# Kernel tuning notes

Hardware: AMD Instinct MI355X
Metric: run time of the kernel (lower is better)

## Reference

```python
import jax, jax.numpy as jnp
import numpy as np

B, T, N, F = 16, 12, 1024, 8
H = 64        # hidden_size
K = 2         # diffusion order (DCRNN k == DiffConv gnn_kernel)
HORIZON = 12
E = 32 * N    # number of edges


def setup_inputs() -> dict:
    key = jax.random.key(0)
    ks = jax.random.split(key, 16)
    s = 0.05
    inp = {}
    inp['x'] = jax.random.normal(ks[0], (B, T, N, F), jnp.float32)
    inp['edge_index'] = jax.random.randint(ks[1], (2, E), 0, N)
    inp['edge_weight'] = jax.random.uniform(ks[2], (E,), jnp.float32)
    inp['adj'] = jax.random.uniform(ks[3], (N, N), jnp.float32)
    # encoder Linear(F -> H)
    inp['W_enc'] = jax.random.normal(ks[4], (F, H), jnp.float32) * s
    inp['b_enc'] = jnp.zeros((H,), jnp.float32)
    # NodeEmbedding(n_nodes, H)
    inp['node_emb'] = jax.random.normal(ks[5], (N, H), jnp.float32) * s
    # DCRNN gates: DenseGraphConvOrderK(2H -> H), 2 supports x K hops (include_self=False)
    gin = 2 * H * 2 * K
    inp['W_r'] = jax.random.normal(ks[6], (gin, H), jnp.float32) * s
    inp['b_r'] = jnp.zeros((H,), jnp.float32)
    inp['W_u'] = jax.random.normal(ks[7], (gin, H), jnp.float32) * s
    inp['b_u'] = jnp.zeros((H,), jnp.float32)
    inp['W_c'] = jax.random.normal(ks[8], (gin, H), jnp.float32) * s
    inp['b_c'] = jnp.zeros((H,), jnp.float32)
    # DiffConv filters: Linear(H*(2K+1) -> H), root_weight=True, add_backward=True
    din = H * (2 * K + 1)
    inp['W_diff'] = jax.random.normal(ks[9], (din, H), jnp.float32) * s
    inp['b_diff'] = jnp.zeros((H,), jnp.float32)
    # decoder Linear(H -> F*HORIZON)
    inp['W_dec'] = jax.random.normal(ks[10], (H, F * HORIZON), jnp.float32) * s
    inp['b_dec'] = jnp.zeros((F * HORIZON,), jnp.float32)
    return inp


def _dgconv(x, supports, W, b):
    # DenseGraphConvOrderK, include_self=False: for each support, K hop powers, concat on channels.
    feats = []
    for a in supports:  # a: [n, n], row-normalized transition matrix
        x1 = x
        for _ in range(K):
            x1 = jnp.einsum('bvc,wv->bwc', x1, a)
            feats.append(x1)
    return jnp.concatenate(feats, axis=-1) @ W + b


def _forward(x, edge_index, edge_weight, adj, W_enc, b_enc, node_emb,
             W_r, b_r, W_u, b_u, W_c, b_c, W_diff, b_diff, W_dec, b_dec):
    # --- DenseGraphConvOrderK.compute_support: fwd/bwd row-normalized transitions ---
    adj_fwd = adj / adj.sum(1, keepdims=True)
    adjT = adj.T
    adj_bwd = adjT / adjT.sum(1, keepdims=True)
    supports = (adj_fwd, adj_bwd)

    # encoder + node embeddings (broadcast over batch & time)
    x_enc = x @ W_enc + b_enc + node_emb  # [B, T, N, H]

    # --- DenseDCRNN: GRU with diffusion-conv gates, scan over time ---
    def step(h, xt):
        xh = jnp.concatenate([xt, h], axis=-1)                 # [B, N, 2H]
        r = jax.nn.sigmoid(_dgconv(xh, supports, W_r, b_r))    # forget/reset gate
        u = jax.nn.sigmoid(_dgconv(xh, supports, W_u, b_u))    # update gate
        xc = jnp.concatenate([xt, r * h], axis=-1)
        c = jnp.tanh(_dgconv(xc, supports, W_c, b_c))          # candidate
        h_new = u * h + (1.0 - u) * c
        return h_new, None

    h0 = jnp.zeros((B, N, H), x_enc.dtype)
    h, _ = jax.lax.scan(step, h0, jnp.swapaxes(x_enc, 0, 1))   # last state, [B, N, H]

    # --- DiffConv readout on sparse edge list (root + K fwd hops + K bwd hops) ---
    src, dst = edge_index[0], edge_index[1]

    def norm_w(group_idx):
        deg = jax.ops.segment_sum(edge_weight, group_idx, num_segments=N)
        inv = jnp.where(deg > 0, 1.0 / deg, 0.0)
        return edge_weight * inv[group_idx]

    w_fwd = norm_w(dst)  # normalize over target (dim=1)
    w_bwd = norm_w(src)  # flipped edges, normalized over their targets (= src)

    feats = [h]
    for s_, d_, w_ in ((src, dst, w_fwd), (dst, src, w_bwd)):
        xs = h
        for _ in range(K):
            msg = xs[:, s_, :] * w_[None, :, None]             # [B, E, H]
            xs = jnp.zeros_like(h).at[:, d_, :].add(msg)
            feats.append(xs)
    z = jnp.concatenate(feats, axis=-1) @ W_diff + b_diff      # [B, N, H]

    # decoder + rearrange 'b n (t f) -> b t n f'
    out = z @ W_dec + b_dec                                    # [B, N, HORIZON*F]
    return out.reshape(B, N, HORIZON, F).transpose(0, 2, 1, 3) # [B, HORIZON, N, F]


def reference(x, edge_index, edge_weight, adj, W_enc, b_enc, node_emb,
              W_r, b_r, W_u, b_u, W_c, b_c, W_diff, b_diff, W_dec, b_dec):
    return _forward(x, edge_index, edge_weight, adj, W_enc, b_enc, node_emb,
                    W_r, b_r, W_u, b_u, W_c, b_c, W_diff, b_diff, W_dec, b_dec)
```

## Files before the change

kernel.cpp:

```cpp
#include <hip/hip_runtime.h>
#include <math.h>

#define BB 16
#define TT 12
#define NN 1024
#define FF 8
#define HH 64
#define EE 32768
#define DIN 320
#define ODIM 96
#define APAD 40

typedef _Float16 v8h __attribute__((ext_vector_type(8)));
typedef float v4f __attribute__((ext_vector_type(4)));

__device__ __forceinline__ unsigned short f2h(float v) {
    _Float16 h = (_Float16)v;
    unsigned short u;
    __builtin_memcpy(&u, &h, 2);
    return u;
}
__device__ __forceinline__ float h2f(unsigned short u) {
    _Float16 h;
    __builtin_memcpy(&h, &u, 2);
    return (float)h;
}
__device__ __forceinline__ void gl_lds16(const void* g, void* l) {
    __builtin_amdgcn_global_load_lds(
        (const __attribute__((address_space(1))) unsigned int*)g,
        (__attribute__((address_space(3))) unsigned int*)l, 16, 0, 0);
}

__global__ void k_ei_detect(const int* __restrict__ ei_raw, int* __restrict__ flag) {
    __shared__ int s[256];
    s[threadIdx.x] = ei_raw[2 * threadIdx.x + 1];
    __syncthreads();
    for (int st = 128; st > 0; st >>= 1) {
        if (threadIdx.x < st) s[threadIdx.x] |= s[threadIdx.x + st];
        __syncthreads();
    }
    if (threadIdx.x == 0) flag[0] = (s[0] == 0) ? 1 : 0;
}
__global__ void k_ei_norm(const int* __restrict__ ei_raw, const int* __restrict__ flag,
                          int* __restrict__ ei32) {
    int j = blockIdx.x * 256 + threadIdx.x;
    ei32[j] = flag[0] ? ei_raw[2 * j] : ei_raw[j];
}

__global__ void k_rowsum(const float* __restrict__ adj, float* __restrict__ rinv) {
    __shared__ float s[256];
    int i = blockIdx.x;
    float acc = 0.f;
    for (int j = threadIdx.x; j < NN; j += 256) acc += adj[i * NN + j];
    s[threadIdx.x] = acc;
    __syncthreads();
    for (int st = 128; st > 0; st >>= 1) {
        if (threadIdx.x < st) s[threadIdx.x] += s[threadIdx.x + st];
        __syncthreads();
    }
    if (threadIdx.x == 0) rinv[i] = (s[0] != 0.f) ? 1.f / s[0] : 0.f;
}
__global__ void k_colsumP(const float* __restrict__ adj, float* __restrict__ csum) {
    int bi = blockIdx.x;
    int j4 = threadIdx.x * 4;
    float4 acc = {0.f, 0.f, 0.f, 0.f};
    const float* base = adj + (size_t)bi * 16 * NN + j4;
    #pragma unroll
    for (int r = 0; r < 16; r++) {
        float4 v = *(const float4*)(base + (size_t)r * NN);
        acc.x += v.x; acc.y += v.y; acc.z += v.z; acc.w += v.w;
    }
    atomicAdd(&csum[j4 + 0], acc.x);
    atomicAdd(&csum[j4 + 1], acc.y);
    atomicAdd(&csum[j4 + 2], acc.z);
    atomicAdd(&csum[j4 + 3], acc.w);
}
__global__ void k_cinv(const float* __restrict__ csum, float* __restrict__ cinv) {
    int j = blockIdx.x * 256 + threadIdx.x;
    float s = csum[j];
    cinv[j] = (s != 0.f) ? 1.f / s : 0.f;
}

__global__ __launch_bounds__(256) void k_prepA(
        const float* __restrict__ adj, const float* __restrict__ rinv,
        const float* __restrict__ cinv, unsigned short* __restrict__ Mp) {
    int w0 = blockIdx.x * 64, v0 = blockIdx.y * 64;
    __shared__ float T[64][68];
    int row = threadIdx.x >> 2, cs = (threadIdx.x & 3) * 16;
    #pragma unroll
    for (int j = 0; j < 4; j++)
        *(float4*)&T[row][cs + j * 4] = *(const float4*)(adj + (size_t)(w0 + row) * NN + v0 + cs + j * 4);
    __syncthreads();
    {
        float sc = rinv[w0 + row];
        unsigned short h8[16];
        #pragma unroll
        for (int j = 0; j < 16; j++) h8[j] = f2h(T[row][cs + j] * sc);
        size_t ofs = (size_t)(w0 + row) * NN + v0 + cs;
        ((uint4*)(Mp + ofs))[0] = *(uint4*)&h8[0];
        ((uint4*)(Mp + ofs))[1] = *(uint4*)&h8[8];
    }
    {
        float sc = cinv[v0 + row];
        unsigned short h8[16];
        #pragma unroll
        for (int j = 0; j < 16; j++) h8[j] = f2h(T[cs + j][row] * sc);
        size_t ofs = (size_t)2048 * NN + (size_t)(v0 + row) * NN + w0 + cs;
        ((uint4*)(Mp + ofs))[0] = *(uint4*)&h8[0];
        ((uint4*)(Mp + ofs))[1] = *(uint4*)&h8[8];
    }
}

__global__ __launch_bounds__(256) void k_msq(unsigned short* __restrict__ M) {
    int zz = blockIdx.z;
    size_t srcb = (size_t)zz * 2048 * NN;
    size_t dstb = srcb + (size_t)1024 * NN;
    int w0 = blockIdx.x * 64, n0 = blockIdx.y * 64;

    __shared__ unsigned short sA[64 * APAD];
    __shared__ unsigned short sB[64 * APAD];

    int tid = threadIdx.x;
    int lane = tid & 63, wave = tid >> 6;
    int wr = (wave >> 1) * 32, wc = (wave & 1) * 32;
    int l15 = lane & 15, quad = lane >> 4;
    int arow = tid >> 2, akk = (tid & 3) * 8;
    int bkr = tid & 31, bc8 = (tid >> 5) * 8;

    v4f acc[2][2];
    #pragma unroll
    for (int i = 0; i < 2; i++)
        #pragma unroll
        for (int j = 0; j < 2; j++) { acc[i][j][0]=0.f; acc[i][j][1]=0.f; acc[i][j][2]=0.f; acc[i][j][3]=0.f; }

    for (int k0 = 0; k0 < NN; k0 += 32) {
        *(uint4*)&sA[arow * APAD + akk] = *(const uint4*)(M + srcb + (size_t)(w0 + arow) * NN + k0 + akk);
        uint4 bh = *(const uint4*)(M + srcb + (size_t)(k0 + bkr) * NN + n0 + bc8);
        const unsigned short* ph = (const unsigned short*)&bh;
        #pragma unroll
        for (int j = 0; j < 8; j++) sB[(bc8 + j) * APAD + bkr] = ph[j];
        __syncthreads();

        v8h a0 = *(const v8h*)&sA[(wr + l15) * APAD + quad * 8];
        v8h a1 = *(const v8h*)&sA[(wr + 16 + l15) * APAD + quad * 8];
        #pragma unroll
        for (int j = 0; j < 2; j++) {
            v8h bb = *(const v8h*)&sB[(wc + j * 16 + l15) * APAD + quad * 8];
            acc[0][j] = __builtin_amdgcn_mfma_f32_16x16x32_f16(a0, bb, acc[0][j], 0, 0, 0);
            acc[1][j] = __builtin_amdgcn_mfma_f32_16x16x32_f16(a1, bb, acc[1][j], 0, 0, 0);
        }
        __syncthreads();
    }

    #pragma unroll
    for (int i = 0; i < 2; i++)
        #pragma unroll
        for (int j = 0; j < 2; j++) {
            int rb = w0 + wr + i * 16 + quad * 4;
            int cc = n0 + wc + j * 16 + l15;
            #pragma unroll
            for (int rr = 0; rr < 4; rr++)
                M[dstb + (size_t)(rb + rr) * NN + cc] = f2h(acc[i][j][rr]);
        }
}

__global__ void k_m2frag(const unsigned short* __restrict__ P, unsigned short* __restrict__ F) {
    size_t t = (size_t)blockIdx.x * 256 + threadIdx.x;
    int rowloc = (int)(t & 63);
    int kc = (int)((t >> 6) & 127);
    int T = (int)(t >> 13);
    size_t src = ((size_t)(T * 64 + rowloc) * NN) + kc * 8;
    *(uint4*)(F + t * 8) = *(const uint4*)(P + src);
}

__global__ void k_xT(const float* __restrict__ x, unsigned short* __restrict__ XallT) {
    int bx = blockIdx.x;
    int t = bx >> 4, b = bx & 15;
    int tid = threadIdx.x;
    int f = tid & 7, half = tid >> 3;
    const float* xs = x + ((size_t)b * TT + t) * NN * FF + f;
    int n0 = half * 32;
    unsigned short v[32];
    #pragma unroll
    for (int i = 0; i < 32; i++) v[i] = f2h(xs[(size_t)(n0 + i) * FF]);
    unsigned short* dst = XallT + ((size_t)bx * 8 + f) * NN + n0;
    #pragma unroll
    for (int i = 0; i < 4; i++) *(uint4*)(dst + i * 8) = *(uint4*)&v[i * 8];
}
__global__ void k_embT(const float* __restrict__ emb, unsigned short* __restrict__ XallT) {
    int c = blockIdx.x;
    int n0 = threadIdx.x * 4;
    unsigned short v[4];
    #pragma unroll
    for (int j = 0; j < 4; j++) v[j] = f2h(emb[(size_t)(n0 + j) * HH + c]);
    *(uint2*)(XallT + (size_t)(1536 + c) * NN + n0) = *(uint2*)v;
}

__global__ __launch_bounds__(512) void k_hopX(
        const unsigned short* __restrict__ Mf,
        const unsigned short* __restrict__ XallT,
        unsigned short* __restrict__ AX, unsigned short* __restrict__ Eg) {
    int bid = blockIdx.x;
    int rt = bid & 31;
    int y  = bid >> 5;
    int g = rt >> 3;
    int n0 = (rt & 7) * 128;
    int c0 = y * 128;

    __shared__ unsigned short sA[2][16 * 512];
    __shared__ unsigned short sX[2][16 * 512];

    int tid = threadIdx.x;
    int lane = tid & 63, wave = tid >> 6;
    int rh = wave >> 2, cq = wave & 3;
    int l15 = lane & 15, quad = lane >> 4;

    v4f acc[4][2];
    #pragma unroll
    for (int i = 0; i < 4; i++)
        #pragma unroll
        for (int j = 0; j < 2; j++) { acc[i][j][0]=0.f; acc[i][j][1]=0.f; acc[i][j][2]=0.f; acc[i][j][3]=0.f; }

    auto STAGE = [&](int buf, int k0) {
        #pragma unroll
        for (int s = 0; s < 4; s++) {
            int id = wave + s * 8;
            if (id < 16) {
                int ah = id >> 3, kh = (id >> 2) & 1, rf = id & 3;
                const unsigned short* src = Mf +
                    ((size_t)(rt * 2 + ah) * 8192 +
                     (size_t)((k0 >> 3) + kh * 4 + quad) * 64 + rf * 16 + l15) * 8;
                gl_lds16(src, &sA[buf][id * 512]);
            } else {
                int xi = id - 16, cj = xi >> 1, kh = xi & 1;
                const unsigned short* src = XallT +
                    (size_t)(c0 + cj * 16 + l15) * NN + k0 + kh * 32 + quad * 8;
                gl_lds16(src, &sX[buf][xi * 512]);
            }
        }
    };

    STAGE(0, 0);
    STAGE(1, 64);

    int lu = lane * 8;
// ... 41 lines not shown
                }
            }
        }
}

__global__ void k_veg(const float* __restrict__ W_enc,
                      const float* __restrict__ W_r, const float* __restrict__ W_u,
                      const float* __restrict__ W_c, float* __restrict__ Veg) {
    int idx = blockIdx.x * 256 + threadIdx.x;
    int c = idx & 63;
    int gf = (idx >> 6) & 31;
    int G = idx >> 11;
    int g = gf >> 3, f = gf & 7;
    const float* W = (G == 0) ? W_r : ((G == 1) ? W_u : W_c);
    float acc = 0.f;
    for (int c2 = 0; c2 < 64; c2++)
        acc += W_enc[f * HH + c2] * W[(size_t)(g * 128 + c2) * HH + c];
    Veg[idx] = acc;
}

__global__ void k_constE(const unsigned short* __restrict__ Eg, const float* __restrict__ b_enc,
                         const float* __restrict__ W_r, const float* __restrict__ W_u,
                         const float* __restrict__ W_c, float* __restrict__ constE) {
    int G = blockIdx.y;
    int n = blockIdx.x * 4 + (threadIdx.x >> 6);
    int c = threadIdx.x & 63;
    const float* W = (G == 0) ? W_r : ((G == 1) ? W_u : W_c);
    float acc = 0.f;
    for (int g = 0; g < 4; g++)
        for (int c2 = 0; c2 < 64; c2++)
            acc += (h2f(Eg[((size_t)(g << 10) + n) * 64 + c2]) + b_enc[c2]) *
                   W[(size_t)(g * 128 + c2) * HH + c];
    constE[((size_t)G << 16) + (size_t)n * 64 + c] = acc;
}

__global__ void k_wfragH(const float* __restrict__ W_r, const float* __restrict__ W_u,
                         const float* __restrict__ W_c,
                         unsigned short* __restrict__ Fr, unsigned short* __restrict__ Fu,
                         unsigned short* __restrict__ Fc) {
    int idx = blockIdx.x * 256 + threadIdx.x;
    int G = idx >> 14;
    int r = idx & 16383;
    int e = r & 7, l = (r >> 3) & 63;
    int rest = r >> 9;
    int ks = rest & 7, cj = rest >> 3;
    int c = cj * 16 + (l & 15);
    int k = ks * 32 + (l >> 4) * 8 + e;
    int g = k >> 6, c2 = k & 63;
    const float* W = (G == 0) ? W_r : ((G == 1) ? W_u : W_c);
    unsigned short* F = (G == 0) ? Fr : ((G == 1) ? Fu : Fc);
    F[r] = f2h(W[(size_t)(g * 128 + 64 + c2) * HH + c]);
}
__global__ void k_wfragX(const float* __restrict__ Veg, unsigned short* __restrict__ Wx) {
    int idx = blockIdx.x * 256 + threadIdx.x;
    int G = idx >> 11;
    int r = idx & 2047;
    int e = r & 7, l = (r >> 3) & 63;
    int cj = r >> 9;
    int c = cj * 16 + (l & 15);
    int k = (l >> 4) * 8 + e;
    Wx[idx] = f2h(Veg[(size_t)G * 2048 + (size_t)k * 64 + c]);
}

__global__ void k_wfragO(const float* __restrict__ W_diff, const float* __restrict__ W_dec,
                         unsigned short* __restrict__ Wf) {
    int idx = blockIdx.x * 256 + threadIdx.x;
    int e = idx & 7, l = (idx >> 3) & 63;
    int rest = idx >> 9;
    int ks = rest % 10, cj = rest / 10;
    int o = cj * 16 + (l & 15);
    int k = ks * 32 + (l >> 4) * 8 + e;
    float acc = 0.f;
    for (int c = 0; c < 64; c++) acc += W_diff[(size_t)k * HH + c] * W_dec[(size_t)c * ODIM + o];
    Wf[idx] = f2h(acc);
}
__global__ void k_bzd(const float* __restrict__ b_diff, const float* __restrict__ W_dec,
                      const float* __restrict__ b_dec, float* __restrict__ bzd) {
    int o = threadIdx.x;
    float acc = b_dec[o];
    for (int c = 0; c < 64; c++) acc += b_diff[c] * W_dec[(size_t)c * ODIM + o];
    bzd[o] = acc;
}

__global__ __launch_bounds__(512) void k_hopRU(
        const unsigned short* __restrict__ Mf,
        const unsigned short* __restrict__ XhH,
        const unsigned short* __restrict__ AXt,
        const unsigned short* __restrict__ WfrH, const unsigned short* __restrict__ WfuH,
        const unsigned short* __restrict__ Wxr, const unsigned short* __restrict__ Wxu,
        const float* __restrict__ b_r, const float* __restrict__ b_u,
        const float* __restrict__ constE,
        const float* __restrict__ h,
        unsigned short* __restrict__ XhR, float* __restrict__ ubuf) {
    int bid = blockIdx.x;
    int b = bid >> 5, nth = bid & 31;
    int nt = nth >> 1, hb = nth & 1;
    int n0 = nth * 32;

    __shared__ unsigned short S[2][24 * 512];

    int tid = threadIdx.x;
    int lane = tid & 63, wave = tid >> 6;
    int l15 = lane & 15, quad = lane >> 4;
    int g = wave >> 1, rh = wave & 1;

    const unsigned short* Xbase = XhH + (size_t)b * 64 * NN;

    v4f acc[4];
    #pragma unroll
    for (int j = 0; j < 4; j++) { acc[j][0]=0.f; acc[j][1]=0.f; acc[j][2]=0.f; acc[j][3]=0.f; }

    auto STAGE = [&](int buf, int k0) {
        #pragma unroll
        for (int s = 0; s < 3; s++) {
            int id = wave + s * 8;
            if (id < 16) {
                int gg = id >> 2, kh = (id >> 1) & 1, rfi = id & 1;
                int rf = hb * 2 + rfi;
                const unsigned short* src = Mf +
                    ((size_t)(gg * 16 + nt) * 8192 +
                     (size_t)((k0 >> 3) + kh * 4 + quad) * 64 + rf * 16 + l15) * 8;
                gl_lds16(src, &S[buf][id * 512]);
            } else {
                int xi = id - 16, cj = xi >> 1, kh = xi & 1;
                const unsigned short* src = Xbase +
                    (size_t)(cj * 16 + l15) * NN + k0 + kh * 32 + quad * 8;
                gl_lds16(src, &S[buf][id * 512]);
            }
        }
    };

    STAGE(0, 0);
    STAGE(1, 64);

    int lu = lane * 8;
    for (int kt = 0; kt < 16; kt++) {
        int cur = kt & 1;
        if (kt < 15) asm volatile("s_waitcnt vmcnt(3)" ::: "memory");
        else         asm volatile("s_waitcnt vmcnt(0)" ::: "memory");
        __builtin_amdgcn_s_barrier();
        asm volatile("" ::: "memory");
        #pragma unroll
        for (int kh = 0; kh < 2; kh++) {
            v8h a = *(const v8h*)&S[cur][(g * 4 + kh * 2 + rh) * 512 + lu];
            #pragma unroll
            for (int cj = 0; cj < 4; cj++) {
                v8h bx = *(const v8h*)&S[cur][(16 + cj * 2 + kh) * 512 + lu];
                acc[cj] = __builtin_amdgcn_mfma_f32_16x16x32_f16(a, bx, acc[cj], 0, 0, 0);
            }
        }
        asm volatile("" ::: "memory");
        __builtin_amdgcn_s_barrier();
        asm volatile("" ::: "memory");
        if (kt < 14) STAGE(cur, (kt + 2) * 64);
    }

    unsigned short* Yt = &S[0][0];
    #pragma unroll
    for (int cj = 0; cj < 4; cj++) {
        int col = g * 64 + cj * 16 + l15;
        #pragma unroll
        for (int rr = 0; rr < 4; rr++) {
            int row = rh * 16 + quad * 4 + rr;
            Yt[row * 264 + col] = f2h(acc[cj][rr]);
        }
    }
    __syncthreads();

    int gate = wave >> 2, rw = (wave >> 1) & 1, ch = wave & 1;
    const unsigned short* WH = gate ? WfuH : WfrH;
    const unsigned short* WX = gate ? Wxu : Wxr;
    const float* bias = gate ? b_u : b_r;
    const float* cE = constE + ((size_t)gate << 16);

    v4f acc2[2];
    #pragma unroll
    for (int j = 0; j < 2; j++) { acc2[j][0]=0.f; acc2[j][1]=0.f; acc2[j][2]=0.f; acc2[j][3]=0.f; }

    {
        v8h ax = *(const v8h*)(AXt + ((size_t)(b << 10) + n0 + rw * 16 + l15) * 32 + quad * 8);
        #pragma unroll
        for (int j = 0; j < 2; j++) {
            v8h bf = *(const v8h*)(WX + (size_t)(ch * 2 + j) * 512 + lu);
            acc2[j] = __builtin_amdgcn_mfma_f32_16x16x32_f16(ax, bf, acc2[j], 0, 0, 0);
        }
    }
    #pragma unroll
    for (int ks = 0; ks < 8; ks++) {
        v8h a = *(const v8h*)&Yt[(rw * 16 + l15) * 264 + ks * 32 + quad * 8];
        #pragma unroll
        for (int j = 0; j < 2; j++) {
            v8h bf = *(const v8h*)(WH + (size_t)((ch * 2 + j) * 8 + ks) * 512 + lu);
            acc2[j] = __builtin_amdgcn_mfma_f32_16x16x32_f16(a, bf, acc2[j], 0, 0, 0);
        }
    }

    unsigned short* sT = &S[1][0];
    if (gate == 0) {
        #pragma unroll
        for (int j = 0; j < 2; j++) {
            int c = (ch * 2 + j) * 16 + l15;
            float bb = bias[c];
            #pragma unroll
            for (int rr = 0; rr < 4; rr++) {
                int nl = rw * 16 + quad * 4 + rr;
                size_t row = (size_t)(b << 10) + n0 + nl;
                float pre = acc2[j][rr] + bb + cE[(size_t)(n0 + nl) * 64 + c];
                float r = 1.f / (1.f + expf(-pre));
                sT[c * 36 + nl] = f2h(r * h[row * 64 + c]);
            }
        }
    } else {
        #pragma unroll
        for (int j = 0; j < 2; j++) {
            int c = (ch * 2 + j) * 16 + l15;
            float bb = bias[c];
            #pragma unroll
            for (int rr = 0; rr < 4; rr++) {
                int nl = rw * 16 + quad * 4 + rr;
                size_t row = (size_t)(b << 10) + n0 + nl;
                float pre = acc2[j][rr] + bb + cE[(size_t)(n0 + nl) * 64 + c];
                ubuf[row * 64 + c] = 1.f / (1.f + expf(-pre));
            }
        }
    }
    __syncthreads();
    {
        int c = tid >> 3, n4 = (tid & 7) * 4;
        *(uint2*)(XhR + ((size_t)b * 64 + c) * NN + n0 + n4) = *(uint2*)&sT[c * 36 + n4];
    }
}

__global__ __launch_bounds__(512) void k_hopC(
        const unsigned short* __restrict__ Mf,
        const unsigned short* __restrict__ XhR,
        const unsigned short* __restrict__ AXt,
        const unsigned short* __restrict__ WfcH, const unsigned short* __restrict__ Wxc,
        const float* __restrict__ b_c,
        const float* __restrict__ constE,
        const float* __restrict__ ubuf,
        float* __restrict__ h, unsigned short* __restrict__ XhH) {
    int bid = blockIdx.x;
    int b = bid >> 5, nth = bid & 31;
    int nt = nth >> 1, hb = nth & 1;
    int n0 = nth * 32;

    __shared__ unsigned short S[2][24 * 512];

    int tid = threadIdx.x;
    int lane = tid & 63, wave = tid >> 6;
    int l15 = lane & 15, quad = lane >> 4;
    int g = wave >> 1, rh = wave & 1;

    const unsigned short* Xbase = XhR + (size_t)b * 64 * NN;

    v4f acc[4];
    #pragma unroll
    for (int j = 0; j < 4; j++) { acc[j][0]=0.f; acc[j][1]=0.f; acc[j][2]=0.f; acc[j][3]=0.f; }

    auto STAGE = [&](int buf, int k0) {
        #pragma unroll
        for (int s = 0; s < 3; s++) {
            int id = wave + s * 8;
            if (id < 16) {
                int gg = id >> 2, kh = (id >> 1) & 1, rfi = id & 1;
                int rf = hb * 2 + rfi;
                const unsigned short* src = Mf +
                    ((size_t)(gg * 16 + nt) * 8192 +
                     (size_t)((k0 >> 3) + kh * 4 + quad) * 64 + rf * 16 + l15) * 8;
                gl_lds16(src, &S[buf][id * 512]);
            } else {
                int xi = id - 16, cj = xi >> 1, kh = xi & 1;
                const unsigned short* src = Xbase +
                    (size_t)(cj * 16 + l15) * NN + k0 + kh * 32 + quad * 8;
                gl_lds16(src, &S[buf][id * 512]);
            }
        }
    };

    STAGE(0, 0);
    STAGE(1, 64);

    int lu = lane * 8;
    for (int kt = 0; kt < 16; kt++) {
        int cur = kt & 1;
        if (kt < 15) asm volatile("s_waitcnt vmcnt(3)" ::: "memory");
        else         asm volatile("s_waitcnt vmcnt(0)" ::: "memory");
        __builtin_amdgcn_s_barrier();
        asm volatile("" ::: "memory");
        #pragma unroll
        for (int kh = 0; kh < 2; kh++) {
            v8h a = *(const v8h*)&S[cur][(g * 4 + kh * 2 + rh) * 512 + lu];
            #pragma unroll
            for (int cj = 0; cj < 4; cj++) {
                v8h bx = *(const v8h*)&S[cur][(16 + cj * 2 + kh) * 512 + lu];
                acc[cj] = __builtin_amdgcn_mfma_f32_16x16x32_f16(a, bx, acc[cj], 0, 0, 0);
            }
        }
        asm volatile("" ::: "memory");
        __builtin_amdgcn_s_barrier();
        asm volatile("" ::: "memory");
        if (kt < 14) STAGE(cur, (kt + 2) * 64);
    }

    unsigned short* Yt = &S[0][0];
    #pragma unroll
    for (int cj = 0; cj < 4; cj++) {
        int col = g * 64 + cj * 16 + l15;
        #pragma unroll
        for (int rr = 0; rr < 4; rr++) {
            int row = rh * 16 + quad * 4 + rr;
            Yt[row * 264 + col] = f2h(acc[cj][rr]);
        }
    }
    __syncthreads();

    int ch = wave >> 1, rw = wave & 1;
    const float* cE = constE + ((size_t)2 << 16);

    v4f acc2;
    acc2[0]=0.f; acc2[1]=0.f; acc2[2]=0.f; acc2[3]=0.f;

    {
        v8h ax = *(const v8h*)(AXt + ((size_t)(b << 10) + n0 + rw * 16 + l15) * 32 + quad * 8);
        v8h bf = *(const v8h*)(Wxc + (size_t)ch * 512 + lu);
        acc2 = __builtin_amdgcn_mfma_f32_16x16x32_f16(ax, bf, acc2, 0, 0, 0);
    }
    #pragma unroll
    for (int ks = 0; ks < 8; ks++) {
        v8h a = *(const v8h*)&Yt[(rw * 16 + l15) * 264 + ks * 32 + quad * 8];
        v8h bf = *(const v8h*)(WfcH + (size_t)(ch * 8 + ks) * 512 + lu);
        acc2 = __builtin_amdgcn_mfma_f32_16x16x32_f16(a, bf, acc2, 0, 0, 0);
    }

    unsigned short* sT = &S[1][0];
    {
        int c = ch * 16 + l15;
        float bb = b_c[c];
        #pragma unroll
        for (int rr = 0; rr < 4; rr++) {
            int nl = rw * 16 + quad * 4 + rr;
            size_t row = (size_t)(b << 10) + n0 + nl;
            float pre = acc2[rr] + bb + cE[(size_t)(n0 + nl) * 64 + c];
            float cv = tanhf(pre);
            float u = ubuf[row * 64 + c];
            float hv = h[row * 64 + c];
            float hn = u * hv + (1.f - u) * cv;
            h[row * 64 + c] = hn;
            sT[c * 36 + nl] = f2h(hn);
        }
    }
    __syncthreads();
    {
        int c = tid >> 3, n4 = (tid & 7) * 4;
        *(uint2*)(XhH + ((size_t)b * 64 + c) * NN + n0 + n4) = *(uint2*)&sT[c * 36 + n4];
    }
}

__global__ __launch_bounds__(512) void k_hopA(
        const unsigned short* __restrict__ Mf,
        const unsigned short* __restrict__ Xb,
        unsigned short* __restrict__ Yout, int out_stride, int out_gmul, int out_off) {
    int bid = blockIdx.x;
    int rt = bid & 31;
    int bp = bid >> 5;
    int g = rt >> 3;
    int n0 = (rt & 7) * 128;

    __shared__ unsigned short sA[2][16 * 512];
    __shared__ unsigned short sX[2][16 * 512];

    int tid = threadIdx.x;
    int lane = tid & 63, wave = tid >> 6;
    int rh = wave >> 2, cq = wave & 3;
    int l15 = lane & 15, quad = lane >> 4;

    const unsigned short* Xbase = Xb + (size_t)(bp * 2) * 64 * NN;

    v4f acc[4][2];
    #pragma unroll
    for (int i = 0; i < 4; i++)
        #pragma unroll
        for (int j = 0; j < 2; j++) { acc[i][j][0]=0.f; acc[i][j][1]=0.f; acc[i][j][2]=0.f; acc[i][j][3]=0.f; }

    auto STAGE = [&](int buf, int k0) {
        #pragma unroll
        for (int s = 0; s < 4; s++) {
            int id = wave + s * 8;
            if (id < 16) {
                int ah = id >> 3, kh = (id >> 2) & 1, rf = id & 3;
                const unsigned short* src = Mf +
                    ((size_t)(rt * 2 + ah) * 8192 +
                     (size_t)((k0 >> 3) + kh * 4 + quad) * 64 + rf * 16 + l15) * 8;
                gl_lds16(src, &sA[buf][id * 512]);
            } else {
                int xi = id - 16, cj = xi >> 1, kh = xi & 1;
                const unsigned short* src = Xbase +
                    (size_t)(cj * 16 + l15) * NN + k0 + kh * 32 + quad * 8;
                gl_lds16(src, &sX[buf][xi * 512]);
            }
        }
    };

    STAGE(0, 0);
    STAGE(1, 64);

    int lu = lane * 8;
    for (int kt = 0; kt < 16; kt++) {
        int cur = kt & 1;
        if (kt < 15) asm volatile("s_waitcnt vmcnt(4)" ::: "memory");
        else         asm volatile("s_waitcnt vmcnt(0)" ::: "memory");
        __builtin_amdgcn_s_barrier();
        asm volatile("" ::: "memory");
        #pragma unroll
        for (int kh = 0; kh < 2; kh++) {
            v8h a[4], bx[2];
            #pragma unroll
            for (int rf = 0; rf < 4; rf++)
                a[rf] = *(const v8h*)&sA[cur][(rh * 8 + kh * 4 + rf) * 512 + lu];
            #pragma unroll
            for (int j = 0; j < 2; j++)
                bx[j] = *(const v8h*)&sX[cur][((cq * 2 + j) * 2 + kh) * 512 + lu];
            #pragma unroll
            for (int rf = 0; rf < 4; rf++)
                #pragma unroll
                for (int j = 0; j < 2; j++)
                    acc[rf][j] = __builtin_amdgcn_mfma_f32_16x16x32_f16(a[rf], bx[j], acc[rf][j], 0, 0, 0);
        }
        asm volatile("" ::: "memory");
        __builtin_amdgcn_s_barrier();
        asm volatile("" ::: "memory");
        if (kt < 14) STAGE(cur, (kt + 2) * 64);
    }

    #pragma unroll
    for (int rf = 0; rf < 4; rf++)
        #pragma unroll
        for (int j = 0; j < 2; j++) {
// ... 30 lines not shown
            acc[cj] = __builtin_amdgcn_mfma_f32_16x16x32_f16(a, bf, acc[cj], 0, 0, 0);
        }
    }
    #pragma unroll
    for (int cj = 0; cj < 6; cj++) {
        int o = cj * 16 + l15;
        int t = o >> 3, f = o & 7;
        float bb = bzd[o];
        #pragma unroll
        for (int rr = 0; rr < 4; rr++) {
            int row = row0 + wave * 16 + quad * 4 + rr;
            int b = row >> 10, n = row & 1023;
            out[(((size_t)b * TT + t) * NN + n) * FF + f] = acc[cj][rr] + bb;
        }
    }
}

__global__ void k_deg(const int* __restrict__ ei32, const float* __restrict__ ew,
                      float* __restrict__ degd, float* __restrict__ degs) {
    int e = blockIdx.x * 256 + threadIdx.x;
    float w = ew[e];
    atomicAdd(&degd[ei32[EE + e]], w);
    atomicAdd(&degs[ei32[e]], w);
}
__global__ void k_spadd(const int* __restrict__ ei32, const float* __restrict__ ew,
                        const float* __restrict__ degd, const float* __restrict__ degs,
                        float* __restrict__ temp) {
    int e = blockIdx.x * 256 + threadIdx.x;
    int s = ei32[e], d = ei32[EE + e];
    float w = ew[e];
    float dd = degd[d], ds = degs[s];
    float wfv = dd > 0.f ? w / dd : 0.f;
    float wbv = ds > 0.f ? w / ds : 0.f;
    atomicAdd(&temp[(size_t)d * NN + s], wfv);
    atomicAdd(&temp[(size_t)NN * NN + (size_t)s * NN + d], wbv);
}
__global__ void k_spconv(const float* __restrict__ temp, unsigned short* __restrict__ Mp) {
    size_t i0 = ((size_t)blockIdx.x * 256 + threadIdx.x) * 8;
    size_t dst = (i0 < (size_t)NN * NN) ? i0 : i0 + (size_t)NN * NN;
    unsigned short h8[8];
    #pragma unroll
    for (int j = 0; j < 8; j++) h8[j] = f2h(temp[i0 + j]);
    *(uint4*)(Mp + dst) = *(uint4*)h8;
}

__global__ void k_featd_h(const float* __restrict__ h, unsigned short* __restrict__ featd) {
    size_t idx = (size_t)blockIdx.x * 256 + threadIdx.x;
    size_t row = idx >> 6; int c = (int)(idx & 63);
    featd[row * DIN + c] = f2h(h[idx]);
}

extern "C" void kernel_launch(void* const* d_in, const int* in_sizes, int n_in,
                              void* d_out, int out_size, void* d_ws, size_t ws_size,
                              hipStream_t stream) {
    const float* x      = (const float*)d_in[0];
    const int*   eiraw  = (const int*)  d_in[1];
    const float* ew     = (const float*)d_in[2];
    const float* adj    = (const float*)d_in[3];
    const float* W_enc  = (const float*)d_in[4];
    const float* b_enc  = (const float*)d_in[5];
    const float* emb    = (const float*)d_in[6];
    const float* W_r    = (const float*)d_in[7];
    const float* b_r    = (const float*)d_in[8];
    const float* W_u    = (const float*)d_in[9];
    const float* b_u    = (const float*)d_in[10];
    const float* W_c    = (const float*)d_in[11];
    const float* b_c    = (const float*)d_in[12];
    const float* W_diff = (const float*)d_in[13];
    const float* b_diff = (const float*)d_in[14];
    const float* W_dec  = (const float*)d_in[15];
    const float* b_dec  = (const float*)d_in[16];

    unsigned short* Mf    = (unsigned short*)d_ws;
    unsigned short* XhH   = Mf + (size_t)4096 * NN;
    unsigned short* XhR   = XhH + (size_t)BB * 64 * NN;
    unsigned short* featd = XhR + (size_t)BB * 64 * NN;
    float* h    = (float*)(featd + (size_t)BB * NN * DIN);
    float* ubuf = h + (size_t)BB * NN * HH;
    unsigned short* AXall = (unsigned short*)(ubuf + (size_t)BB * NN * HH);
    unsigned short* Mp    = AXall;
    unsigned short* XallT = AXall + (size_t)192 * NN * 32;
    unsigned short* Eg    = XallT + (size_t)1600 * NN;
    float* sptmp  = (float*)(Eg + (size_t)4 * NN * 64);
    float* constE = sptmp + (size_t)2 * NN * NN;
    float* Veg    = constE + (size_t)3 * NN * 64;
    unsigned short* WfH  = (unsigned short*)(Veg + 3 * 32 * 64);
    unsigned short* WfrH = WfH;
    unsigned short* WfuH = WfH + 16384;
    unsigned short* WfcH = WfH + 32768;
    unsigned short* Wx   = WfH + 49152;
    unsigned short* Wf_o = Wx + 6144;
    float* bzd  = (float*)(Wf_o + 30720);
    float* rinv = bzd + ODIM;
    float* cinv = rinv + NN;
    int*   eifl = (int*)(cinv + NN);
    int*   ei32 = eifl + 4;
    float* degd = (float*)(ei32 + 2 * EE);
    float* degs = degd + NN;
    float* csum = degs + NN;

    hipMemsetAsync(h, 0, (size_t)BB * NN * HH * 4, stream);
    hipMemsetAsync(XhH, 0, (size_t)BB * 64 * NN * 2, stream);
    hipMemsetAsync(csum, 0, NN * 4, stream);

    k_rowsum<<<NN, 256, 0, stream>>>(adj, rinv);
    k_colsumP<<<64, 256, 0, stream>>>(adj, csum);
    k_cinv<<<NN / 256, 256, 0, stream>>>(csum, cinv);
    k_prepA<<<dim3(16, 16), 256, 0, stream>>>(adj, rinv, cinv, Mp);
    k_msq<<<dim3(16, 16, 2), 256, 0, stream>>>(Mp);
    k_m2frag<<<2048, 256, 0, stream>>>(Mp, Mf);

    k_xT<<<TT * BB, 256, 0, stream>>>(x, XallT);
    k_embT<<<64, 256, 0, stream>>>(emb, XallT);
    k_hopX<<<13 * 32, 512, 0, stream>>>(Mf, XallT, AXall, Eg);
    k_veg<<<24, 256, 0, stream>>>(W_enc, W_r, W_u, W_c, Veg);
    k_constE<<<dim3(256, 3), 256, 0, stream>>>(Eg, b_enc, W_r, W_u, W_c, constE);
    k_wfragH<<<192, 256, 0, stream>>>(W_r, W_u, W_c, WfrH, WfuH, WfcH);
    k_wfragX<<<24, 256, 0, stream>>>(Veg, Wx);
    k_wfragO<<<120, 256, 0, stream>>>(W_diff, W_dec, Wf_o);
    k_bzd<<<1, ODIM, 0, stream>>>(b_diff, W_dec, b_dec, bzd);

    for (int t = 0; t < TT; t++) {
        const unsigned short* AXt = AXall + (size_t)t * BB * NN * 32;
        k_hopRU<<<512, 512, 0, stream>>>(Mf, XhH, AXt, WfrH, WfuH, Wx, Wx + 2048,
                                         b_r, b_u, constE, h, XhR, ubuf);
        k_hopC<<<512, 512, 0, stream>>>(Mf, XhR, AXt, WfcH, Wx + 4096,
                                        b_c, constE, ubuf, h, XhH);
    }

    k_ei_detect<<<1, 256, 0, stream>>>(eiraw, eifl);
    k_ei_norm<<<2 * EE / 256, 256, 0, stream>>>(eiraw, eifl, ei32);
    hipMemsetAsync(degd, 0, (size_t)2 * NN * 4, stream);
    hipMemsetAsync(sptmp, 0, (size_t)2 * NN * NN * 4, stream);
    k_deg<<<EE / 256, 256, 0, stream>>>(ei32, ew, degd, degs);
    k_spadd<<<EE / 256, 256, 0, stream>>>(ei32, ew, degd, degs, sptmp);
    k_spconv<<<2 * NN * NN / (256 * 8), 256, 0, stream>>>(sptmp, Mp);
    k_msq<<<dim3(16, 16, 2), 256, 0, stream>>>(Mp);
    k_m2frag<<<2048, 256, 0, stream>>>(Mp, Mf);
    k_featd_h<<<BB * NN * HH / 256, 256, 0, stream>>>(h, featd);
    k_hopA<<<8 * 32, 512, 0, stream>>>(Mf, XhH, featd, DIN, 64, 64);
    k_out<<<BB * NN / 64, 256, 0, stream>>>(featd, Wf_o, bzd, (float*)d_out);
}
```

Before: 722.1 us.

## Retile matrix-square GEMM with pre-transposed B and halve recurrent hop block size

Replaces the naive LDS-staged matrix-square kernel with a separate transpose pass followed by a 128x128-tile, double-buffered, direct-to-LDS MFMA GEMM. This removes the scattered transposing LDS stores and raises per-wave reuse. The recurrent hopRU/hopC kernels drop from 512 to 256 threads per block, with each wave now computing two row fragments, so register reuse per wave goes up. The trade-off is fewer waves available to hide latency, plus an extra transpose kernel and scratch buffer that aliases sptmp.

Result: slower. 753.8 us (+4.4%).

```diff
diff --git a/kernel.cpp b/kernel.cpp
--- a/kernel.cpp
+++ b/kernel.cpp
@@ -9,7 +9,6 @@
 #define EE 32768
 #define DIN 320
 #define ODIM 96
-#define APAD 40
 
 typedef _Float16 v8h __attribute__((ext_vector_type(8)));
 typedef float v4f __attribute__((ext_vector_type(4)));
@@ -111,56 +110,104 @@
     }
 }
 
-__global__ __launch_bounds__(256) void k_msq(unsigned short* __restrict__ M) {
+__global__ __launch_bounds__(256) void k_mT(const unsigned short* __restrict__ Mp,
+                                            unsigned short* __restrict__ Mt) {
     int zz = blockIdx.z;
-    size_t srcb = (size_t)zz * 2048 * NN;
-    size_t dstb = srcb + (size_t)1024 * NN;
-    int w0 = blockIdx.x * 64, n0 = blockIdx.y * 64;
-
-    __shared__ unsigned short sA[64 * APAD];
-    __shared__ unsigned short sB[64 * APAD];
+    int r0 = blockIdx.x * 64, c0 = blockIdx.y * 64;
+    __shared__ unsigned short T[64][72];
+    int row = threadIdx.x >> 2, cs = (threadIdx.x & 3) * 16;
+    const unsigned short* src = Mp + (size_t)zz * 2048 * NN + (size_t)(r0 + row) * NN + c0 + cs;
+    *(uint4*)&T[row][cs] = *(const uint4*)src;
+    *(uint4*)&T[row][cs + 8] = *(const uint4*)(src + 8);
+    __syncthreads();
+    unsigned short v[16];
+    #pragma unroll
+    for (int j = 0; j < 16; j++) v[j] = T[cs + j][row];
+    unsigned short* dst = Mt + (size_t)zz * 1024 * NN + (size_t)(c0 + row) * NN + r0 + cs;
+    *(uint4*)dst = *(uint4*)&v[0];
+    *(uint4*)(dst + 8) = *(uint4*)&v[8];
+}
+
+__global__ __launch_bounds__(512) void k_msq2(unsigned short* __restrict__ M,
+                                              const unsigned short* __restrict__ Mt) {
+    int bid = blockIdx.x;
+    int zz = bid >> 6, t = bid & 63;
+    int r0 = (t >> 3) * 128, c0 = (t & 7) * 128;
+    size_t asec = (size_t)zz * 2048 * NN;
+    const unsigned short* Arows = M + asec;
+    const unsigned short* Brows = Mt + (size_t)zz * 1024 * NN;
+    unsigned short* D = M + asec + (size_t)1024 * NN;
+
+    __shared__ unsigned short sA[2][16 * 512];
+    __shared__ unsigned short sB[2][16 * 512];
 
     int tid = threadIdx.x;
     int lane = tid & 63, wave = tid >> 6;
-    int wr = (wave >> 1) * 32, wc = (wave & 1) * 32;
+    int rh = wave >> 2, cq = wave & 3;
     int l15 = lane & 15, quad = lane >> 4;
-    int arow = tid >> 2, akk = (tid & 3) * 8;
-    int bkr = tid & 31, bc8 = (tid >> 5) * 8;
-
-    v4f acc[2][2];
-    #pragma unroll
-    for (int i = 0; i < 2; i++)
+
+    v4f acc[4][2];
+    #pragma unroll
+    for (int i = 0; i < 4; i++)
         #pragma unroll
         for (int j = 0; j < 2; j++) { acc[i][j][0]=0.f; acc[i][j][1]=0.f; acc[i][j][2]=0.f; acc[i][j][3]=0.f; }
 
-    for (int k0 = 0; k0 < NN; k0 += 32) {
-        *(uint4*)&sA[arow * APAD + akk] = *(const uint4*)(M + srcb + (size_t)(w0 + arow) * NN + k0 + akk);
-        uint4 bh = *(const uint4*)(M + srcb + (size_t)(k0 + bkr) * NN + n0 + bc8);
-        const unsigned short* ph = (const unsigned short*)&bh;
-        #pragma unroll
-        for (int j = 0; j < 8; j++) sB[(bc8 + j) * APAD + bkr] = ph[j];
-        __syncthreads();
-
-        v8h a0 = *(const v8h*)&sA[(wr + l15) * APAD + quad * 8];
-        v8h a1 = *(const v8h*)&sA[(wr + 16 + l15) * APAD + quad * 8];
+    auto STAGE = [&](int buf, int k0) {
+        #pragma unroll
+        for (int s = 0; s < 4; s++) {
+            int id = wave + s * 8;
+            if (id < 16) {
+                int rf = id >> 1, kh = id & 1;
+                const unsigned short* src = Arows + (size_t)(r0 + rf * 16 + l15) * NN + k0 + kh * 32 + quad * 8;
+                gl_lds16(src, &sA[buf][id * 512]);
+            } else {
+                int xi = id - 16, cj = xi >> 1, kh = xi & 1;
+                const unsigned short* src = Brows + (size_t)(c0 + cj * 16 + l15) * NN + k0 + kh * 32 + quad * 8;
+                gl_lds16(src, &sB[buf][xi * 512]);
+            }
+        }
+    };
+
+    STAGE(0, 0);
+    STAGE(1, 64);
+
+    int lu = lane * 8;
+    for (int kt = 0; kt < 16; kt++) {
+        int cur = kt & 1;
+        if (kt < 15) asm volatile("s_waitcnt vmcnt(4)" ::: "memory");
+        else         asm volatile("s_waitcnt vmcnt(0)" ::: "memory");
+        __builtin_amdgcn_s_barrier();
+        asm volatile("" ::: "memory");
+        #pragma unroll
+        for (int kh = 0; kh < 2; kh++) {
+            v8h a[4], bx[2];
+            #pragma unroll
+            for (int i = 0; i < 4; i++)
+                a[i] = *(const v8h*)&sA[cur][((rh * 4 + i) * 2 + kh) * 512 + lu];
+            #pragma unroll
+            for (int j = 0; j < 2; j++)
+                bx[j] = *(const v8h*)&sB[cur][((cq * 2 + j) * 2 + kh) * 512 + lu];
+            #pragma unroll
+            for (int i = 0; i < 4; i++)
+                #pragma unroll
+                for (int j = 0; j < 2; j++)
+                    acc[i][j] = __builtin_amdgcn_mfma_f32_16x16x32_f16(a[i], bx[j], acc[i][j], 0, 0, 0);
+        }
+        asm volatile("" ::: "memory");
+        __builtin_amdgcn_s_barrier();
+        asm volatile("" ::: "memory");
+        if (kt < 14) STAGE(cur, (kt + 2) * 64);
+    }
+
+    #pragma unroll
+    for (int rf = 0; rf < 4; rf++)
         #pragma unroll
         for (int j = 0; j < 2; j++) {
-            v8h bb = *(const v8h*)&sB[(wc + j * 16 + l15) * APAD + quad * 8];
-            acc[0][j] = __builtin_amdgcn_mfma_f32_16x16x32_f16(a0, bb, acc[0][j], 0, 0, 0);
-            acc[1][j] = __builtin_amdgcn_mfma_f32_16x16x32_f16(a1, bb, acc[1][j], 0, 0, 0);
-        }
-        __syncthreads();
-    }
-
-    #pragma unroll
-    for (int i = 0; i < 2; i++)
-        #pragma unroll
-        for (int j = 0; j < 2; j++) {
-            int rb = w0 + wr + i * 16 + quad * 4;
-            int cc = n0 + wc + j * 16 + l15;
+            int row = r0 + rh * 64 + rf * 16 + quad * 4;
+            int col = c0 + cq * 32 + j * 16 + l15;
             #pragma unroll
             for (int rr = 0; rr < 4; rr++)
-                M[dstb + (size_t)(rb + rr) * NN + cc] = f2h(acc[i][j][rr]);
+                D[(size_t)(row + rr) * NN + col] = f2h(acc[rf][j][rr]);
         }
 }
 
@@ -368,7 +415,7 @@
     bzd[o] = acc;
 }
 
-__global__ __launch_bounds__(512) void k_hopRU(
+__global__ __launch_bounds__(256) void k_hopRU(
         const unsigned short* __restrict__ Mf,
         const unsigned short* __restrict__ XhH,
         const unsigned short* __restrict__ AXt,
@@ -386,20 +433,21 @@
     __shared__ unsigned short S[2][24 * 512];
 
     int tid = threadIdx.x;
-    int lane = tid & 63, wave = tid >> 6;
+    int lane = tid & 63, g = tid >> 6;
     int l15 = lane & 15, quad = lane >> 4;
-    int g = wave >> 1, rh = wave & 1;
 
     const unsigned short* Xbase = XhH + (size_t)b * 64 * NN;
 
-    v4f acc[4];
-    #pragma unroll
-    for (int j = 0; j < 4; j++) { acc[j][0]=0.f; acc[j][1]=0.f; acc[j][2]=0.f; acc[j][3]=0.f; }
+    v4f acc[2][4];
+    #pragma unroll
+    for (int i = 0; i < 2; i++)
+        #pragma unroll
+        for (int j = 0; j < 4; j++) { acc[i][j][0]=0.f; acc[i][j][1]=0.f; acc[i][j][2]=0.f; acc[i][j][3]=0.f; }
 
     auto STAGE = [&](int buf, int k0) {
         #pragma unroll
-        for (int s = 0; s < 3; s++) {
-            int id = wave + s * 8;
+        for (int s = 0; s < 6; s++) {
+            int id = g + s * 4;
             if (id < 16) {
                 int gg = id >> 2, kh = (id >> 1) & 1, rfi = id & 1;
                 int rf = hb * 2 + rfi;
@@ -422,17 +470,21 @@
     int lu = lane * 8;
     for (int kt = 0; kt < 16; kt++) {
         int cur = kt & 1;
-        if (kt < 15) asm volatile("s_waitcnt vmcnt(3)" ::: "memory");
+        if (kt < 15) asm volatile("s_waitcnt vmcnt(6)" ::: "memory");
         else         asm volatile("s_waitcnt vmcnt(0)" ::: "memory");
         __builtin_amdgcn_s_barrier();
         asm volatile("" ::: "memory");
         #pragma unroll
         for (int kh = 0; kh < 2; kh++) {
-            v8h a = *(const v8h*)&S[cur][(g * 4 + kh * 2 + rh) * 512 + lu];
+            v8h a[2];
+            #pragma unroll
+            for (int i = 0; i < 2; i++)
+                a[i] = *(const v8h*)&S[cur][(g * 4 + kh * 2 + i) * 512 + lu];
             #pragma unroll
             for (int cj = 0; cj < 4; cj++) {
                 v8h bx = *(const v8h*)&S[cur][(16 + cj * 2 + kh) * 512 + lu];
-                acc[cj] = __builtin_amdgcn_mfma_f32_16x16x32_f16(a, bx, acc[cj], 0, 0, 0);
+                acc[0][cj] = __builtin_amdgcn_mfma_f32_16x16x32_f16(a[0], bx, acc[0][cj], 0, 0, 0);
+                acc[1][cj] = __builtin_amdgcn_mfma_f32_16x16x32_f16(a[1], bx, acc[1][cj], 0, 0, 0);
             }
         }
         asm volatile("" ::: "memory");
@@ -443,81 +495,92 @@
 
     unsigned short* Yt = &S[0][0];
     #pragma unroll
-    for (int cj = 0; cj < 4; cj++) {
-        int col = g * 64 + cj * 16 + l15;
-        #pragma unroll
-        for (int rr = 0; rr < 4; rr++) {
-            int row = rh * 16 + quad * 4 + rr;
-            Yt[row * 264 + col] = f2h(acc[cj][rr]);
-        }
-    }
+    for (int i = 0; i < 2; i++)
+        #pragma unroll
+        for (int cj = 0; cj < 4; cj++) {
+            int col = g * 64 + cj * 16 + l15;
+            #pragma unroll
+            for (int rr = 0; rr < 4; rr++) {
+                int row = i * 16 + quad * 4 + rr;
+                Yt[row * 264 + col] = f2h(acc[i][cj][rr]);
+            }
+        }
     __syncthreads();
 
-    int gate = wave >> 2, rw = (wave >> 1) & 1, ch = wave & 1;
+    int gate = g >> 1, ch = g & 1;
     const unsigned short* WH = gate ? WfuH : WfrH;
     const unsigned short* WX = gate ? Wxu : Wxr;
     const float* bias = gate ? b_u : b_r;
     const float* cE = constE + ((size_t)gate << 16);
 
-    v4f acc2[2];
-    #pragma unroll
-    for (int j = 0; j < 2; j++) { acc2[j][0]=0.f; acc2[j][1]=0.f; acc2[j][2]=0.f; acc2[j][3]=0.f; }
-
-    {
-        v8h ax = *(const v8h*)(AXt + ((size_t)(b << 10) + n0 + rw * 16 + l15) * 32 + quad * 8);
+    v4f acc2[2][2];
+    #pragma unroll
+    for (int i = 0; i < 2; i++)
+        #pragma unroll
+        for (int j = 0; j < 2; j++) { acc2[i][j][0]=0.f; acc2[i][j][1]=0.f; acc2[i][j][2]=0.f; acc2[i][j][3]=0.f; }
+
+    #pragma unroll
+    for (int i = 0; i < 2; i++) {
+        v8h ax = *(const v8h*)(AXt + ((size_t)(b << 10) + n0 + i * 16 + l15) * 32 + quad * 8);
         #pragma unroll
         for (int j = 0; j < 2; j++) {
             v8h bf = *(const v8h*)(WX + (size_t)(ch * 2 + j) * 512 + lu);
-            acc2[j] = __builtin_amdgcn_mfma_f32_16x16x32_f16(ax, bf, acc2[j], 0, 0, 0);
+            acc2[i][j] = __builtin_amdgcn_mfma_f32_16x16x32_f16(ax, bf, acc2[i][j], 0, 0, 0);
         }
     }
     #pragma unroll
     for (int ks = 0; ks < 8; ks++) {
-        v8h a = *(const v8h*)&Yt[(rw * 16 + l15) * 264 + ks * 32 + quad * 8];
+        v8h a0 = *(const v8h*)&Yt[(l15) * 264 + ks * 32 + quad * 8];
+        v8h a1 = *(const v8h*)&Yt[(16 + l15) * 264 + ks * 32 + quad * 8];
         #pragma unroll
         for (int j = 0; j < 2; j++) {
             v8h bf = *(const v8h*)(WH + (size_t)((ch * 2 + j) * 8 + ks) * 512 + lu);
-            acc2[j] = __builtin_amdgcn_mfma_f32_16x16x32_f16(a, bf, acc2[j], 0, 0, 0);
+            acc2[0][j] = __builtin_amdgcn_mfma_f32_16x16x32_f16(a0, bf, acc2[0][j], 0, 0, 0);
+            acc2[1][j] = __builtin_amdgcn_mfma_f32_16x16x32_f16(a1, bf, acc2[1][j], 0, 0, 0);
         }
     }
 
     unsigned short* sT = &S[1][0];
     if (gate == 0) {
         #pragma unroll
-        for (int j = 0; j < 2; j++) {
-            int c = (ch * 2 + j) * 16 + l15;
-            float bb = bias[c];
-            #pragma unroll
-            for (int rr = 0; rr < 4; rr++) {
-                int nl = rw * 16 + quad * 4 + rr;
-                size_t row = (size_t)(b << 10) + n0 + nl;
-                float pre = acc2[j][rr] + bb + cE[(size_t)(n0 + nl) * 64 + c];
-                float r = 1.f / (1.f + expf(-pre));
-                sT[c * 36 + nl] = f2h(r * h[row * 64 + c]);
-            }
-        }
+        for (int i = 0; i < 2; i++)
+            #pragma unroll
+            for (int j = 0; j < 2; j++) {
+                int c = (ch * 2 + j) * 16 + l15;
+                float bb = bias[c];
+                #pragma unroll
+                for (int rr = 0; rr < 4; rr++) {
+                    int nl = i * 16 + quad * 4 + rr;
+                    size_t row = (size_t)(b << 10) + n0 + nl;
+                    float pre = acc2[i][j][rr] + bb + cE[(size_t)(n0 + nl) * 64 + c];
+                    float r = 1.f / (1.f + expf(-pre));
+                    sT[c * 36 + nl] = f2h(r * h[row * 64 + c]);
+                }
+            }
     } else {
         #pragma unroll
-        for (int j = 0; j < 2; j++) {
-            int c = (ch * 2 + j) * 16 + l15;
-            float bb = bias[c];
-            #pragma unroll
-            for (int rr = 0; rr < 4; rr++) {
-                int nl = rw * 16 + quad * 4 + rr;
-                size_t row = (size_t)(b << 10) + n0 + nl;
-                float pre = acc2[j][rr] + bb + cE[(size_t)(n0 + nl) * 64 + c];
-                ubuf[row * 64 + c] = 1.f / (1.f + expf(-pre));
-            }
-        }
+        for (int i = 0; i < 2; i++)
+            #pragma unroll
+            for (int j = 0; j < 2; j++) {
+                int c = (ch * 2 + j) * 16 + l15;
+                float bb = bias[c];
+                #pragma unroll
+                for (int rr = 0; rr < 4; rr++) {
+                    int nl = i * 16 + quad * 4 + rr;
+                    size_t row = (size_t)(b << 10) + n0 + nl;
+                    float pre = acc2[i][j][rr] + bb + cE[(size_t)(n0 + nl) * 64 + c];
+                    ubuf[row * 64 + c] = 1.f / (1.f + expf(-pre));
+                }
+            }
     }
     __syncthreads();
     {
-        int c = tid >> 3, n4 = (tid & 7) * 4;
-        *(uint2*)(XhR + ((size_t)b * 64 + c) * NN + n0 + n4) = *(uint2*)&sT[c * 36 + n4];
-    }
-}
-
-__global__ __launch_bounds__(512) void k_hopC(
+        int c = tid >> 2, n8 = (tid & 3) * 8;
+        *(uint4*)(XhR + ((size_t)b * 64 + c) * NN + n0 + n8) = *(uint4*)&sT[c * 36 + n8];
+    }
+}
+
+__global__ __launch_bounds__(256) void k_hopC(
         const unsigned short* __restrict__ Mf,
         const unsigned short* __restrict__ XhR,
         const unsigned short* __restrict__ AXt,
@@ -534,20 +597,21 @@
     __shared__ unsigned short S[2][24 * 512];
 
     int tid = threadIdx.x;
-    int lane = tid & 63, wave = tid >> 6;
+    int lane = tid & 63, g = tid >> 6;
     int l15 = lane & 15, quad = lane >> 4;
-    int g = wave >> 1, rh = wave & 1;
 
     const unsigned short* Xbase = XhR + (size_t)b * 64 * NN;
 
-    v4f acc[4];
-    #pragma unroll
-    for (int j = 0; j < 4; j++) { acc[j][0]=0.f; acc[j][1]=0.f; acc[j][2]=0.f; acc[j][3]=0.f; }
+    v4f acc[2][4];
+    #pragma unroll
+    for (int i = 0; i < 2; i++)
+        #pragma unroll
+        for (int j = 0; j < 4; j++) { acc[i][j][0]=0.f; acc[i][j][1]=0.f; acc[i][j][2]=0.f; acc[i][j][3]=0.f; }
 
     auto STAGE = [&](int buf, int k0) {
         #pragma unroll
-        for (int s = 0; s < 3; s++) {
-            int id = wave + s * 8;
+        for (int s = 0; s < 6; s++) {
+            int id = g + s * 4;
             if (id < 16) {
                 int gg = id >> 2, kh = (id >> 1) & 1, rfi = id & 1;
                 int rf = hb * 2 + rfi;
@@ -570,17 +634,21 @@
     int lu = lane * 8;
     for (int kt = 0; kt < 16; kt++) {
         int cur = kt & 1;
-        if (kt < 15) asm volatile("s_waitcnt vmcnt(3)" ::: "memory");
+        if (kt < 15) asm volatile("s_waitcnt vmcnt(6)" ::: "memory");
         else         asm volatile("s_waitcnt vmcnt(0)" ::: "memory");
         __builtin_amdgcn_s_barrier();
         asm volatile("" ::: "memory");
         #pragma unroll
         for (int kh = 0; kh < 2; kh++) {
-            v8h a = *(const v8h*)&S[cur][(g * 4 + kh * 2 + rh) * 512 + lu];
+            v8h a[2];
+            #pragma unroll
+            for (int i = 0; i < 2; i++)
+                a[i] = *(const v8h*)&S[cur][(g * 4 + kh * 2 + i) * 512 + lu];
             #pragma unroll
             for (int cj = 0; cj < 4; cj++) {
                 v8h bx = *(const v8h*)&S[cur][(16 + cj * 2 + kh) * 512 + lu];
-                acc[cj] = __builtin_amdgcn_mfma_f32_16x16x32_f16(a, bx, acc[cj], 0, 0, 0);
+                acc[0][cj] = __builtin_amdgcn_mfma_f32_16x16x32_f16(a[0], bx, acc[0][cj], 0, 0, 0);
+                acc[1][cj] = __builtin_amdgcn_mfma_f32_16x16x32_f16(a[1], bx, acc[1][cj], 0, 0, 0);
             }
         }
         asm volatile("" ::: "memory");
@@ -591,32 +659,38 @@
 
     unsigned short* Yt = &S[0][0];
     #pragma unroll
-    for (int cj = 0; cj < 4; cj++) {
-        int col = g * 64 + cj * 16 + l15;
-        #pragma unroll
-        for (int rr = 0; rr < 4; rr++) {
-            int row = rh * 16 + quad * 4 + rr;
-            Yt[row * 264 + col] = f2h(acc[cj][rr]);
-        }
-    }
+    for (int i = 0; i < 2; i++)
+        #pragma unroll
+        for (int cj = 0; cj < 4; cj++) {
+            int col = g * 64 + cj * 16 + l15;
+            #pragma unroll
+            for (int rr = 0; rr < 4; rr++) {
+                int row = i * 16 + quad * 4 + rr;
+                Yt[row * 264 + col] = f2h(acc[i][cj][rr]);
+            }
+        }
     __syncthreads();
 
-    int ch = wave >> 1, rw = wave & 1;
+    int ch = g;
     const float* cE = constE + ((size_t)2 << 16);
 
-    v4f acc2;
-    acc2[0]=0.f; acc2[1]=0.f; acc2[2]=0.f; acc2[3]=0.f;
-
-    {
-        v8h ax = *(const v8h*)(AXt + ((size_t)(b << 10) + n0 + rw * 16 + l15) * 32 + quad * 8);
+    v4f acc2[2];
+    #pragma unroll
+    for (int i = 0; i < 2; i++) { acc2[i][0]=0.f; acc2[i][1]=0.f; acc2[i][2]=0.f; acc2[i][3]=0.f; }
+
+    #pragma unroll
+    for (int i = 0; i < 2; i++) {
+        v8h ax = *(const v8h*)(AXt + ((size_t)(b << 10) + n0 + i * 16 + l15) * 32 + quad * 8);
         v8h bf = *(const v8h*)(Wxc + (size_t)ch * 512 + lu);
-        acc2 = __builtin_amdgcn_mfma_f32_16x16x32_f16(ax, bf, acc2, 0, 0, 0);
+        acc2[i] = __builtin_amdgcn_mfma_f32_16x16x32_f16(ax, bf, acc2[i], 0, 0, 0);
     }
     #pragma unroll
     for (int ks = 0; ks < 8; ks++) {
-        v8h a = *(const v8h*)&Yt[(rw * 16 + l15) * 264 + ks * 32 + quad * 8];
+        v8h a0 = *(const v8h*)&Yt[(l15) * 264 + ks * 32 + quad * 8];
+        v8h a1 = *(const v8h*)&Yt[(16 + l15) * 264 + ks * 32 + quad * 8];
         v8h bf = *(const v8h*)(WfcH + (size_t)(ch * 8 + ks) * 512 + lu);
-        acc2 = __builtin_amdgcn_mfma_f32_16x16x32_f16(a, bf, acc2, 0, 0, 0);
+        acc2[0] = __builtin_amdgcn_mfma_f32_16x16x32_f16(a0, bf, acc2[0], 0, 0, 0);
+        acc2[1] = __builtin_amdgcn_mfma_f32_16x16x32_f16(a1, bf, acc2[1], 0, 0, 0);
     }
 
     unsigned short* sT = &S[1][0];
@@ -624,22 +698,24 @@
         int c = ch * 16 + l15;
         float bb = b_c[c];
         #pragma unroll
-        for (int rr = 0; rr < 4; rr++) {
-            int nl = rw * 16 + quad * 4 + rr;
-            size_t row = (size_t)(b << 10) + n0 + nl;
-            float pre = acc2[rr] + bb + cE[(size_t)(n0 + nl) * 64 + c];
-            float cv = tanhf(pre);
-            float u = ubuf[row * 64 + c];
-            float hv = h[row * 64 + c];
-            float hn = u * hv + (1.f - u) * cv;
-            h[row * 64 + c] = hn;
-            sT[c * 36 + nl] = f2h(hn);
-        }
+        for (int i = 0; i < 2; i++)
+            #pragma unroll
+            for (int rr = 0; rr < 4; rr++) {
+                int nl = i * 16 + quad * 4 + rr;
+                size_t row = (size_t)(b << 10) + n0 + nl;
+                float pre = acc2[i][rr] + bb + cE[(size_t)(n0 + nl) * 64 + c];
+                float cv = tanhf(pre);
+                float u = ubuf[row * 64 + c];
+                float hv = h[row * 64 + c];
+                float hn = u * hv + (1.f - u) * cv;
+                h[row * 64 + c] = hn;
+                sT[c * 36 + nl] = f2h(hn);
+            }
     }
     __syncthreads();
     {
-        int c = tid >> 3, n4 = (tid & 7) * 4;
-        *(uint2*)(XhH + ((size_t)b * 64 + c) * NN + n0 + n4) = *(uint2*)&sT[c * 36 + n4];
+        int c = tid >> 2, n8 = (tid & 3) * 8;
+        *(uint4*)(XhH + ((size_t)b * 64 + c) * NN + n0 + n8) = *(uint4*)&sT[c * 36 + n8];
     }
 }
 
@@ -836,6 +912,7 @@
     unsigned short* XallT = AXall + (size_t)192 * NN * 32;
     unsigned short* Eg    = XallT + (size_t)1600 * NN;
     float* sptmp  = (float*)(Eg + (size_t)4 * NN * 64);
+    unsigned short* Mt = (unsigned short*)sptmp;
     float* constE = sptmp + (size_t)2 * NN * NN;
     float* Veg    = constE + (size_t)3 * NN * 64;
     unsigned short* WfH  = (unsigned short*)(Veg + 3 * 32 * 64);
@@ -861,7 +938,8 @@
     k_colsumP<<<64, 256, 0, stream>>>(adj, csum);
     k_cinv<<<NN / 256, 256, 0, stream>>>(csum, cinv);
     k_prepA<<<dim3(16, 16), 256, 0, stream>>>(adj, rinv, cinv, Mp);
-    k_msq<<<dim3(16, 16, 2), 256, 0, stream>>>(Mp);
+    k_mT<<<dim3(16, 16, 2), 256, 0, stream>>>(Mp, Mt);
+    k_msq2<<<128, 512, 0, stream>>>(Mp, Mt);
     k_m2frag<<<2048, 256, 0, stream>>>(Mp, Mf);
 
     k_xT<<<TT * BB, 256, 0, stream>>>(x, XallT);
@@ -876,9 +954,9 @@
 
     for (int t = 0; t < TT; t++) {
         const unsigned short* AXt = AXall + (size_t)t * BB * NN * 32;
-        k_hopRU<<<512, 512, 0, stream>>>(Mf, XhH, AXt, WfrH, WfuH, Wx, Wx + 2048,
+        k_hopRU<<<512, 256, 0, stream>>>(Mf, XhH, AXt, WfrH, WfuH, Wx, Wx + 2048,
                                          b_r, b_u, constE, h, XhR, ubuf);
-        k_hopC<<<512, 512, 0, stream>>>(Mf, XhR, AXt, WfcH, Wx + 4096,
+        k_hopC<<<512, 256, 0, stream>>>(Mf, XhR, AXt, WfcH, Wx + 4096,
                                         b_c, constE, ubuf, h, XhH);
     }
 
@@ -889,7 +967,8 @@
     k_deg<<<EE / 256, 256, 0, stream>>>(ei32, ew, degd, degs);
     k_spadd<<<EE / 256, 256, 0, stream>>>(ei32, ew, degd, degs, sptmp);
     k_spconv<<<2 * NN * NN / (256 * 8), 256, 0, stream>>>(sptmp, Mp);
-    k_msq<<<dim3(16, 16, 2), 256, 0, stream>>>(Mp);
+    k_mT<<<dim3(16, 16, 2), 256, 0, stream>>>(Mp, Mt);
+    k_msq2<<<128, 512, 0, stream>>>(Mp, Mt);
     k_m2frag<<<2048, 256, 0, stream>>>(Mp, Mf);
     k_featd_h<<<BB * NN * HH / 256, 256, 0, stream>>>(h, featd);
     k_hopA<<<8 * 32, 512, 0, stream>>>(Mf, XhH, featd, DIN, 64, 64);
```
